# Performance work log

Measured on AMD Instinct MI355X. Metric: run time of the kernel, lower is better.

Reference implementation:

```python
import jax, jax.numpy as jnp
import numpy as np

DIM = 512
HEADS = 8
NUM_KEYS = 256
TOPK = 32
DIM_HEAD = 128
LN_EPS = 1e-5


def setup_inputs() -> dict:
    key = jax.random.key(0)
    k1, k2, k3, k4 = jax.random.split(key, 4)
    b, t = 2, 1024
    dim_query = DIM_HEAD * HEADS * 2
    x = jax.random.normal(k1, (b, t, DIM), dtype=jnp.float32)
    # nn.Linear(dim, dim_query, bias=False): weight (dim_query, dim), default kaiming-ish; use scaled normal
    Wq = jax.random.normal(k2, (dim_query, DIM), dtype=jnp.float32) / np.sqrt(DIM)
    # keys: (heads, num_keys, 2, dim_head), std = 1/sqrt(dim_head)
    keys = jax.random.normal(k3, (HEADS, NUM_KEYS, 2, DIM_HEAD), dtype=jnp.float32) / np.sqrt(DIM_HEAD)
    # values: (num_keys**2, dim), std = 1/sqrt(dim)
    values = jax.random.normal(k4, (NUM_KEYS ** 2, DIM), dtype=jnp.float32) / np.sqrt(DIM)
    ln_gamma = jnp.ones((DIM_HEAD,), dtype=jnp.float32)
    ln_beta = jnp.zeros((DIM_HEAD,), dtype=jnp.float32)
    return {"x": x, "Wq": Wq, "keys": keys, "values": values,
            "ln_gamma": ln_gamma, "ln_beta": ln_beta}


def reference(x, Wq, keys, values, ln_gamma, ln_beta):
    b, t, _ = x.shape
    h, n, _, d = keys.shape  # (heads, num_keys, 2, dim_head)
    k = TOPK

    # queries: 'b t (p h d)' -> (b, t, 2, h, d)
    q = jnp.einsum('btc,qc->btq', x, Wq).reshape(b, t, 2, h, d)

    # LayerNorm over dim_head (use_layernorm=True path)
    mu = q.mean(axis=-1, keepdims=True)
    var = q.var(axis=-1, keepdims=True)
    q = (q - mu) * jax.lax.rsqrt(var + LN_EPS) * ln_gamma + ln_beta

    # dots: 'p b t h d, h n p d -> b t h p n'
    dots = jnp.einsum('btphd,hnpd->bthpn', q, keys)

    # top-k per sub-key half: (b, t, h, 2, k)
    scores, indices = jax.lax.top_k(dots, k)
    sx, sy = scores[..., 0, :], scores[..., 1, :]
    ix, iy = indices[..., 0, :], indices[..., 1, :]

    # outer combination -> (b, t, h, k*k)
    all_scores = (sx[..., :, None] + sy[..., None, :]).reshape(b, t, h, k * k)
    all_indices = (ix[..., :, None] * n + iy[..., None, :]).reshape(b, t, h, k * k)

    final_scores, final_idx = jax.lax.top_k(all_scores, k)  # (b, t, h, k)
    value_indices = jnp.take_along_axis(all_indices, final_idx, axis=-1)
    attn = jax.nn.softmax(final_scores, axis=-1)

    vi = value_indices.reshape(b * t, h * k)
    w = attn.reshape(b * t, h * k)

    # EmbeddingBag(mode='sum') with per-sample weights
    gathered = values[vi]                      # (bt, hk, dim)
    out = jnp.einsum('nkd,nk->nd', gathered, w)
    return out.reshape(b, t, -1)
```

## Files before the change

kernel.cpp:

```cpp
#include <hip/hip_runtime.h>
#include <math.h>

#define DQ 2048
#define CDIM 512
#define NKEYS 256
#define KSEL 32

__device__ __forceinline__ bool rank_before(float as, int ai, float bs, int bi) {
  return (as > bs) || (as == bs && ai < bi);
}
static __device__ __forceinline__ float bf2f(unsigned int u) {
  union { unsigned int i; float f; } v; v.i = u << 16; return v.f;
}
static __device__ __forceinline__ unsigned int f2bf(float f) {
  union { float f; unsigned int i; } v; v.f = f;
  unsigned int r = v.i + 0x7fffu + ((v.i >> 16) & 1u);
  return r >> 16;
}

__global__ __launch_bounds__(256) void qgemm_ln(
    const float* __restrict__ X, const float* __restrict__ W,
    const float* __restrict__ gamma, const float* __restrict__ beta,
    float* __restrict__ Q) {
  __shared__ float As[16 * 68];
  __shared__ float Bs[16 * 132];
  const int tid = threadIdx.x;
  const int m0 = blockIdx.x * 64, n0 = blockIdx.y * 128;
  const int tx = tid & 15, ty = tid >> 4;
  const int am = tid >> 2, ak = (tid & 3) * 4;
  const int bn = tid >> 1, bk = (tid & 1) * 8;
  float acc[4][8] = {};
  float4 av  = *(const float4*)&X[(size_t)(m0 + am) * CDIM + ak];
  float4 bv0 = *(const float4*)&W[(size_t)(n0 + bn) * CDIM + bk];
  float4 bv1 = *(const float4*)&W[(size_t)(n0 + bn) * CDIM + bk + 4];
  for (int kt = 0; kt < CDIM; kt += 16) {
    __syncthreads();
    As[(ak + 0) * 68 + am] = av.x; As[(ak + 1) * 68 + am] = av.y;
    As[(ak + 2) * 68 + am] = av.z; As[(ak + 3) * 68 + am] = av.w;
    Bs[(bk + 0) * 132 + bn] = bv0.x; Bs[(bk + 1) * 132 + bn] = bv0.y;
    Bs[(bk + 2) * 132 + bn] = bv0.z; Bs[(bk + 3) * 132 + bn] = bv0.w;
    Bs[(bk + 4) * 132 + bn] = bv1.x; Bs[(bk + 5) * 132 + bn] = bv1.y;
    Bs[(bk + 6) * 132 + bn] = bv1.z; Bs[(bk + 7) * 132 + bn] = bv1.w;
    __syncthreads();
    if (kt + 16 < CDIM) {
      av  = *(const float4*)&X[(size_t)(m0 + am) * CDIM + kt + 16 + ak];
      bv0 = *(const float4*)&W[(size_t)(n0 + bn) * CDIM + kt + 16 + bk];
      bv1 = *(const float4*)&W[(size_t)(n0 + bn) * CDIM + kt + 16 + bk + 4];
    }
    #pragma unroll
    for (int kk = 0; kk < 16; ++kk) {
      float4 a4  = *(const float4*)&As[kk * 68 + ty * 4];
      float4 b4a = *(const float4*)&Bs[kk * 132 + tx * 8];
      float4 b4b = *(const float4*)&Bs[kk * 132 + tx * 8 + 4];
      const float ar[4] = {a4.x, a4.y, a4.z, a4.w};
      const float br[8] = {b4a.x, b4a.y, b4a.z, b4a.w, b4b.x, b4b.y, b4b.z, b4b.w};
      #pragma unroll
      for (int i = 0; i < 4; ++i)
        #pragma unroll
        for (int j = 0; j < 8; ++j)
          acc[i][j] += ar[i] * br[j];
    }
  }
  float g[8], bta[8];
  #pragma unroll
  for (int j = 0; j < 8; ++j) { g[j] = gamma[tx * 8 + j]; bta[j] = beta[tx * 8 + j]; }
  #pragma unroll
  for (int i = 0; i < 4; ++i) {
    float s = 0.f, sq = 0.f;
    #pragma unroll
    for (int j = 0; j < 8; ++j) { s += acc[i][j]; sq += acc[i][j] * acc[i][j]; }
    #pragma unroll
    for (int m = 1; m < 16; m <<= 1) {
      s += __shfl_xor(s, m, 64);
      sq += __shfl_xor(sq, m, 64);
    }
    float mean = s * (1.0f / 128.0f);
    float var = sq * (1.0f / 128.0f) - mean * mean;
    float rs = 1.0f / sqrtf(var + 1e-5f);
    float o[8];
    #pragma unroll
    for (int j = 0; j < 8; ++j) o[j] = (acc[i][j] - mean) * rs * g[j] + bta[j];
    float* dst = &Q[(size_t)(m0 + ty * 4 + i) * DQ + n0 + tx * 8];
    *(float4*)dst = make_float4(o[0], o[1], o[2], o[3]);
    *(float4*)(dst + 4) = make_float4(o[4], o[5], o[6], o[7]);
  }
}

__global__ __launch_bounds__(512, 5) void dots_sel(
    const float* __restrict__ Q, const float* __restrict__ keys,
    float* __restrict__ s1s, int* __restrict__ s1i) {
  const int hp = blockIdx.x;
  const int chunk = blockIdx.y;
  const int h = hp >> 1, p = hp & 1;
  const int t0 = chunk * 32;
  __shared__ float Qs[32 * 132];
  __shared__ float Bs[16 * 260];
  const int tid = threadIdx.x;
  const int w = tid >> 6, lane = tid & 63;
  {
    const int tok = tid >> 4, d0 = (tid & 15) * 8;
    const float* src = &Q[(size_t)(t0 + tok) * DQ + p * 1024 + h * 128 + d0];
    *(float4*)&Qs[tok * 132 + d0] = *(const float4*)src;
    *(float4*)&Qs[tok * 132 + d0 + 4] = *(const float4*)(src + 4);
  }
  const int bn = tid >> 1, bkh = (tid & 1) * 8;
  const float* kbase = keys + ((size_t)(h * NKEYS + bn) * 2 + p) * 128;
  float acc[4][4] = {};
  float4 b0 = *(const float4*)&kbase[bkh];
  float4 b1 = *(const float4*)&kbase[bkh + 4];
  for (int kt = 0; kt < 128; kt += 16) {
    __syncthreads();
    Bs[(bkh + 0) * 260 + bn] = b0.x; Bs[(bkh + 1) * 260 + bn] = b0.y;
    Bs[(bkh + 2) * 260 + bn] = b0.z; Bs[(bkh + 3) * 260 + bn] = b0.w;
    Bs[(bkh + 4) * 260 + bn] = b1.x; Bs[(bkh + 5) * 260 + bn] = b1.y;
    Bs[(bkh + 6) * 260 + bn] = b1.z; Bs[(bkh + 7) * 260 + bn] = b1.w;
    __syncthreads();
    if (kt + 16 < 128) {
      b0 = *(const float4*)&kbase[kt + 16 + bkh];
      b1 = *(const float4*)&kbase[kt + 16 + bkh + 4];
    }
    #pragma unroll
    for (int k4 = 0; k4 < 16; k4 += 4) {
      float4 a0 = *(const float4*)&Qs[(w * 4 + 0) * 132 + kt + k4];
      float4 a1 = *(const float4*)&Qs[(w * 4 + 1) * 132 + kt + k4];
      float4 a2 = *(const float4*)&Qs[(w * 4 + 2) * 132 + kt + k4];
      float4 a3 = *(const float4*)&Qs[(w * 4 + 3) * 132 + kt + k4];
      const float a0r[4] = {a0.x, a0.y, a0.z, a0.w};
      const float a1r[4] = {a1.x, a1.y, a1.z, a1.w};
      const float a2r[4] = {a2.x, a2.y, a2.z, a2.w};
      const float a3r[4] = {a3.x, a3.y, a3.z, a3.w};
      #pragma unroll
      for (int kk = 0; kk < 4; ++kk) {
        float4 b4 = *(const float4*)&Bs[(k4 + kk) * 260 + lane * 4];
        const float br[4] = {b4.x, b4.y, b4.z, b4.w};
        #pragma unroll
        for (int j = 0; j < 4; ++j) {
          acc[0][j] += a0r[kk] * br[j];
          acc[1][j] += a1r[kk] * br[j];
          acc[2][j] += a2r[kk] * br[j];
          acc[3][j] += a3r[kk] * br[j];
        }
      }
    }
  }
  #define CE1(S, I, a, b, dd)                                                  \
    {                                                                          \
      bool sw_ = (dd) ? rank_before(S[a], I[a], S[b], I[b])                    \
                      : rank_before(S[b], I[b], S[a], I[a]);                   \
      if (sw_) {                                                               \
        float ts_ = S[a]; S[a] = S[b]; S[b] = ts_;                             \
        int ti_ = I[a]; I[a] = I[b]; I[b] = ti_;                               \
      }                                                                        \
    }
  #define CEP(a, b, dd) { CE1(sA, iA, a, b, dd) CE1(sB, iB, a, b, dd) }
  #define CROSSP(L, dd)                                                        \
    {                                                                          \
      bool amHigh = (lane & (L)) != 0;                                         \
      bool flip = amHigh != (dd);                                              \
      _Pragma("unroll")                                                        \
      for (int r = 0; r < 4; ++r) {                                            \
        float osA = __shfl_xor(sA[r], (L), 64);                                \
        int oiA = __shfl_xor(iA[r], (L), 64);                                  \
        float osB = __shfl_xor(sB[r], (L), 64);                                \
        int oiB = __shfl_xor(iB[r], (L), 64);                                  \
        bool tA = rank_before(osA, oiA, sA[r], iA[r]) != flip;                 \
        if (tA) { sA[r] = osA; iA[r] = oiA; }                                  \
        bool tB = rank_before(osB, oiB, sB[r], iB[r]) != flip;                 \
        if (tB) { sB[r] = osB; iB[r] = oiB; }                                  \
      }                                                                        \
    }
  #pragma unroll
  for (int ii = 0; ii < 4; ii += 2) {
    float sA[4], sB[4]; int iA[4], iB[4];
    #pragma unroll
    for (int r = 0; r < 4; ++r) {
      sA[r] = acc[ii][r];     iA[r] = lane * 4 + r;
      sB[r] = acc[ii + 1][r]; iB[r] = lane * 4 + r;
    }
    CEP(0, 1, false); CEP(2, 3, true);
    {
      bool dd = (lane & 1) != 0;
      CEP(0, 2, dd); CEP(1, 3, dd); CEP(0, 1, dd); CEP(2, 3, dd);
    }
    #pragma unroll
    for (int K = 8; K <= 256; K <<= 1) {
      bool dd = (lane & (K >> 2)) != 0;
      #pragma unroll
      for (int L = K >> 3; L >= 1; L >>= 1) CROSSP(L, dd);
      CEP(0, 2, dd); CEP(1, 3, dd); CEP(0, 1, dd); CEP(2, 3, dd);
    }
    const int instA = (t0 + w * 4 + ii) * 16 + hp;
    const int instB = instA + 16;
    if (lane < 8) {
      *(float4*)&s1s[(size_t)instA * KSEL + lane * 4] = make_float4(sA[0], sA[1], sA[2], sA[3]);
      *(int4*)&s1i[(size_t)instA * KSEL + lane * 4] = make_int4(iA[0], iA[1], iA[2], iA[3]);
      *(float4*)&s1s[(size_t)instB * KSEL + lane * 4] = make_float4(sB[0], sB[1], sB[2], sB[3]);
      *(int4*)&s1i[(size_t)instB * KSEL + lane * 4] = make_int4(iB[0], iB[1], iB[2], iB[3]);
    }
  }
  #undef CE1
  #undef CEP
  #undef CROSSP
}

__constant__ unsigned short slot_ij[128] = {
  0,1,2,3,4,5,6,7,8,9,10,11,12,13,14,15,16,17,18,19,20,21,22,23,24,25,26,27,28,29,30,31,
  32,33,34,35,36,37,38,39,40,41,42,43,44,45,46,47,
  64,65,66,67,68,69,70,71,72,73,
  96,97,98,99,100,101,102,103,
  128,129,130,131,132,133,
  160,161,162,163,164,
  192,193,194,195,
  224,225,226,227,
  256,257,258,
  288,289,290,
  320,321, 352,353, 384,385, 416,417, 448,449, 480,481,
  512,544,576,608,640,672,704,736,768,800,832,864,896,928,960,992,
  0xFFFF,0xFFFF,0xFFFF,0xFFFF,0xFFFF,0xFFFF,0xFFFF,0xFFFF,0xFFFF
};

__global__ __launch_bounds__(256) void stage2_kernel(
    const float* __restrict__ s1s, const int* __restrict__ s1i,
    float* __restrict__ wgt, int* __restrict__ vidx) {
  const int th = blockIdx.x * 4 + (threadIdx.x >> 6);
  const int lane = threadIdx.x & 63;
  const int bx = th * 64;
  const int by = bx + 32;
  float s[2]; int id[2];
  #pragma unroll
  for (int r = 0; r < 2; ++r) {
    int sl = slot_ij[lane * 2 + r];
    if (sl != 0xFFFF) {
      s[r] = s1s[bx + (sl >> 5)] + s1s[by + (sl & 31)];
      id[r] = sl;
    } else {
      s[r] = -INFINITY; id[r] = 0x7fffffff;
    }
  }
  #define CE2(dd)                                                              \
    {                                                                          \
      bool sw = (dd) ? rank_before(s[0], id[0], s[1], id[1])                   \
                     : rank_before(s[1], id[1], s[0], id[0]);                  \
      if (sw) {                                                                \
        float ts = s[0]; s[0] = s[1]; s[1] = ts;                               \
        int ti = id[0]; id[0] = id[1]; id[1] = ti;                             \
      }                                                                        \
    }
  #define CROSS2(L, dd)                                                        \
    {                                                                          \
      bool amHigh = (lane & (L)) != 0;                                         \
      bool flip = amHigh != (dd);                                              \
      _Pragma("unroll")                                                        \
      for (int r = 0; r < 2; ++r) {                                            \
        float os = __shfl_xor(s[r], (L), 64);                                  \
        int oi = __shfl_xor(id[r], (L), 64);                                   \
        bool take = rank_before(os, oi, s[r], id[r]) != flip;                  \
        if (take) { s[r] = os; id[r] = oi; }                                   \
      }                                                                        \
    }
  { bool dd = (lane & 1) != 0; CE2(dd); }
  #pragma unroll
  for (int K = 4; K <= 128; K <<= 1) {
    bool dd = (lane & (K >> 1)) != 0;
    #pragma unroll
    for (int L = K >> 2; L >= 1; L >>= 1) CROSS2(L, dd);
    CE2(dd);
  }
  #undef CE2
  #undef CROSS2
  float smax = __shfl(s[0], 0, 64);
  float e0 = 0.f, e1 = 0.f;
  if (lane < 16) { e0 = expf(s[0] - smax); e1 = expf(s[1] - smax); }
  float part = e0 + e1;
  #pragma unroll
  for (int m = 1; m < 16; m <<= 1) part += __shfl_xor(part, m, 64);
  if (lane < 16) {
    int f0 = id[0], f1 = id[1];
    int vi0 = s1i[bx + (f0 >> 5)] * NKEYS + s1i[by + (f0 & 31)];
    int vi1 = s1i[bx + (f1 >> 5)] * NKEYS + s1i[by + (f1 & 31)];
    wgt[(size_t)th * KSEL + lane * 2] = e0 / part;
    wgt[(size_t)th * KSEL + lane * 2 + 1] = e1 / part;
    vidx[(size_t)th * KSEL + lane * 2] = vi0;
    vidx[(size_t)th * KSEL + lane * 2 + 1] = vi1;
  }
}

__global__ __launch_bounds__(256) void convert_values(
    const float* __restrict__ values, unsigned int* __restrict__ vbf) {
  const size_t g = ((size_t)blockIdx.x * 256 + threadIdx.x) * 8;
  float4 a = *(const float4*)(values + g);
  float4 b = *(const float4*)(values + g + 4);
  uint4 pk;
  pk.x = f2bf(a.x) | (f2bf(a.y) << 16);
  pk.y = f2bf(a.z) | (f2bf(a.w) << 16);
  pk.z = f2bf(b.x) | (f2bf(b.y) << 16);
  pk.w = f2bf(b.z) | (f2bf(b.w) << 16);
  *(uint4*)(vbf + g / 2) = pk;
}

__global__ __launch_bounds__(256) void gather_bf16(
    const float* __restrict__ wgt, const int* __restrict__ vidx,
    const unsigned short* __restrict__ vbf, float* __restrict__ out) {
  const int t = blockIdx.x;
  const int tid = threadIdx.x, w = tid >> 6, lane = tid & 63;
  __shared__ float ws_[256];
  __shared__ int vs_[256];
  __shared__ float part[4 * 520];
  ws_[tid] = wgt[(size_t)t * 256 + tid];
  vs_[tid] = vidx[(size_t)t * 256 + tid];
  __syncthreads();
  float acc[8] = {};
  const int c0 = lane * 8;
  #pragma unroll 1
  for (int phase = 0; phase < 4; ++phase) {
    for (int e = w; e < 256; e += 4) {
      const int row = vs_[e];
      if ((row >> 14) != phase) continue;
      const float wv = ws_[e];
      uint4 pk = *(const uint4*)(vbf + (size_t)row * CDIM + c0);
      acc[0] += wv * bf2f(pk.x & 0xffff); acc[1] += wv * bf2f(pk.x >> 16);
      acc[2] += wv * bf2f(pk.y & 0xffff); acc[3] += wv * bf2f(pk.y >> 16);
      acc[4] += wv * bf2f(pk.z & 0xffff); acc[5] += wv * bf2f(pk.z >> 16);
      acc[6] += wv * bf2f(pk.w & 0xffff); acc[7] += wv * bf2f(pk.w >> 16);
    }
  }
  #pragma unroll
  for (int j = 0; j < 8; j += 4)
    *(float4*)&part[w * 520 + c0 + j] =
        make_float4(acc[j], acc[j + 1], acc[j + 2], acc[j + 3]);
  __syncthreads();
  const int c2 = tid * 2;
  float r0 = part[c2] + part[520 + c2] + part[1040 + c2] + part[1560 + c2];
  float r1 = part[c2 + 1] + part[520 + c2 + 1] + part[1040 + c2 + 1] + part[1560 + c2 + 1];
  *(float2*)(out + (size_t)t * CDIM + c2) = make_float2(r0, r1);
}

__global__ __launch_bounds__(256) void gather_kernel(
    const float* __restrict__ wgt, const int* __restrict__ vidx,
    const float* __restrict__ values, float* __restrict__ out) {
  const int tp = blockIdx.x;
  const int tid = threadIdx.x;
  __shared__ float ws_[512];
  __shared__ int vs_[512];
  ws_[tid] = wgt[(size_t)tp * 512 + tid];
  ws_[tid + 256] = wgt[(size_t)tp * 512 + tid + 256];
  vs_[tid] = vidx[(size_t)tp * 512 + tid];
  vs_[tid + 256] = vidx[(size_t)tp * 512 + tid + 256];
  __syncthreads();
  const int sub = tid >> 7;
  const int c4 = (tid & 127) * 4;
  const float* wp = &ws_[sub * 256];
  const int* vp = &vs_[sub * 256];
  float4 a = make_float4(0.f, 0.f, 0.f, 0.f);
  #pragma unroll 4
  for (int e = 0; e < 256; ++e) {
    float4 vv = *(const float4*)(values + (size_t)vp[e] * CDIM + c4);
    float wv = wp[e];
    a.x += wv * vv.x; a.y += wv * vv.y; a.z += wv * vv.z; a.w += wv * vv.w;
  }
  *(float4*)(out + (size_t)(tp * 2 + sub) * CDIM + c4) = a;
}

extern "C" void kernel_launch(void* const* d_in, const int* in_sizes, int n_in,
                              void* d_out, int out_size, void* d_ws, size_t ws_size,
                              hipStream_t stream) {
  const float* X      = (const float*)d_in[0];
  const float* W      = (const float*)d_in[1];
  const float* keys   = (const float*)d_in[2];
  const float* values = (const float*)d_in[3];
  const float* gamma  = (const float*)d_in[4];
  const float* beta   = (const float*)d_in[5];
  char* ws = (char*)d_ws;
  float* s1s = (float*)(ws);
  int*   s1i = (int*)  (ws + (4u << 20));
  float* wgt = (float*)(ws + (8u << 20));
  int*   vix = (int*)  (ws + (10u << 20));
  float* Q   = (float*)(ws + (12u << 20));
  unsigned int* vbf = (unsigned int*)(ws + (12u << 20));

  const bool bf16_path = ws_size >= (76u << 20);

  qgemm_ln<<<dim3(32, 16), 256, 0, stream>>>(X, W, gamma, beta, Q);
  dots_sel<<<dim3(16, 64), 512, 0, stream>>>(Q, keys, s1s, s1i);
  stage2_kernel<<<4096, 256, 0, stream>>>(s1s, s1i, wgt, vix);
  if (bf16_path) {
    convert_values<<<16384, 256, 0, stream>>>(values, vbf);
    gather_bf16<<<2048, 256, 0, stream>>>(wgt, vix, (const unsigned short*)vbf, (float*)d_out);
  } else {
    gather_kernel<<<1024, 256, 0, stream>>>(wgt, vix, values, (float*)d_out);
  }
}
```

Baseline: 454.9 us.

## Pre-transpose keys and read them directly from global memory in dots_sel

```diff
diff --git a/kernel.cpp b/kernel.cpp
--- a/kernel.cpp
+++ b/kernel.cpp
@@ -86,15 +86,46 @@
   }
 }
 
+__global__ __launch_bounds__(256) void transpose_keys(
+    const float* __restrict__ keys, float* __restrict__ keysT) {
+  __shared__ float tile[64 * 129];
+  const int hp = blockIdx.x, h = hp >> 1, p = hp & 1;
+  const int n0 = blockIdx.y * 64;
+  {
+    const int n = threadIdx.x >> 2;
+    const int d0 = (threadIdx.x & 3) * 32;
+    const float* src = &keys[(((size_t)h * NKEYS + n0 + n) * 2 + p) * 128 + d0];
+    #pragma unroll
+    for (int j = 0; j < 32; j += 4) {
+      float4 v = *(const float4*)(src + j);
+      tile[n * 129 + d0 + j + 0] = v.x;
+      tile[n * 129 + d0 + j + 1] = v.y;
+      tile[n * 129 + d0 + j + 2] = v.z;
+      tile[n * 129 + d0 + j + 3] = v.w;
+    }
+  }
+  __syncthreads();
+  {
+    const int d = threadIdx.x >> 1;
+    const int nh = (threadIdx.x & 1) * 32;
+    float* dst = &keysT[((size_t)hp * 128 + d) * NKEYS + n0 + nh];
+    #pragma unroll
+    for (int j = 0; j < 32; j += 4) {
+      float4 o = make_float4(tile[(nh + j + 0) * 129 + d], tile[(nh + j + 1) * 129 + d],
+                             tile[(nh + j + 2) * 129 + d], tile[(nh + j + 3) * 129 + d]);
+      *(float4*)(dst + j) = o;
+    }
+  }
+}
+
 __global__ __launch_bounds__(512, 5) void dots_sel(
-    const float* __restrict__ Q, const float* __restrict__ keys,
+    const float* __restrict__ Q, const float* __restrict__ keysT,
     float* __restrict__ s1s, int* __restrict__ s1i) {
   const int hp = blockIdx.x;
   const int chunk = blockIdx.y;
   const int h = hp >> 1, p = hp & 1;
   const int t0 = chunk * 32;
   __shared__ float Qs[32 * 132];
-  __shared__ float Bs[16 * 260];
   const int tid = threadIdx.x;
   const int w = tid >> 6, lane = tid & 63;
   {
@@ -103,43 +134,29 @@
     *(float4*)&Qs[tok * 132 + d0] = *(const float4*)src;
     *(float4*)&Qs[tok * 132 + d0 + 4] = *(const float4*)(src + 4);
   }
-  const int bn = tid >> 1, bkh = (tid & 1) * 8;
-  const float* kbase = keys + ((size_t)(h * NKEYS + bn) * 2 + p) * 128;
+  __syncthreads();
+  const float* kT = keysT + (size_t)hp * 128 * NKEYS + lane * 4;
   float acc[4][4] = {};
-  float4 b0 = *(const float4*)&kbase[bkh];
-  float4 b1 = *(const float4*)&kbase[bkh + 4];
-  for (int kt = 0; kt < 128; kt += 16) {
-    __syncthreads();
-    Bs[(bkh + 0) * 260 + bn] = b0.x; Bs[(bkh + 1) * 260 + bn] = b0.y;
-    Bs[(bkh + 2) * 260 + bn] = b0.z; Bs[(bkh + 3) * 260 + bn] = b0.w;
-    Bs[(bkh + 4) * 260 + bn] = b1.x; Bs[(bkh + 5) * 260 + bn] = b1.y;
-    Bs[(bkh + 6) * 260 + bn] = b1.z; Bs[(bkh + 7) * 260 + bn] = b1.w;
-    __syncthreads();
-    if (kt + 16 < 128) {
-      b0 = *(const float4*)&kbase[kt + 16 + bkh];
-      b1 = *(const float4*)&kbase[kt + 16 + bkh + 4];
-    }
-    #pragma unroll
-    for (int k4 = 0; k4 < 16; k4 += 4) {
-      float4 a0 = *(const float4*)&Qs[(w * 4 + 0) * 132 + kt + k4];
-      float4 a1 = *(const float4*)&Qs[(w * 4 + 1) * 132 + kt + k4];
-      float4 a2 = *(const float4*)&Qs[(w * 4 + 2) * 132 + kt + k4];
-      float4 a3 = *(const float4*)&Qs[(w * 4 + 3) * 132 + kt + k4];
-      const float a0r[4] = {a0.x, a0.y, a0.z, a0.w};
-      const float a1r[4] = {a1.x, a1.y, a1.z, a1.w};
-      const float a2r[4] = {a2.x, a2.y, a2.z, a2.w};
-      const float a3r[4] = {a3.x, a3.y, a3.z, a3.w};
+  #pragma unroll 2
+  for (int kt = 0; kt < 128; kt += 4) {
+    float4 a0 = *(const float4*)&Qs[(w * 4 + 0) * 132 + kt];
+    float4 a1 = *(const float4*)&Qs[(w * 4 + 1) * 132 + kt];
+    float4 a2 = *(const float4*)&Qs[(w * 4 + 2) * 132 + kt];
+    float4 a3 = *(const float4*)&Qs[(w * 4 + 3) * 132 + kt];
+    const float a0r[4] = {a0.x, a0.y, a0.z, a0.w};
+    const float a1r[4] = {a1.x, a1.y, a1.z, a1.w};
+    const float a2r[4] = {a2.x, a2.y, a2.z, a2.w};
+    const float a3r[4] = {a3.x, a3.y, a3.z, a3.w};
+    #pragma unroll
+    for (int kk = 0; kk < 4; ++kk) {
+      float4 b4 = *(const float4*)&kT[(size_t)(kt + kk) * NKEYS];
+      const float br[4] = {b4.x, b4.y, b4.z, b4.w};
       #pragma unroll
-      for (int kk = 0; kk < 4; ++kk) {
-        float4 b4 = *(const float4*)&Bs[(k4 + kk) * 260 + lane * 4];
-        const float br[4] = {b4.x, b4.y, b4.z, b4.w};
-        #pragma unroll
-        for (int j = 0; j < 4; ++j) {
-          acc[0][j] += a0r[kk] * br[j];
-          acc[1][j] += a1r[kk] * br[j];
-          acc[2][j] += a2r[kk] * br[j];
-          acc[3][j] += a3r[kk] * br[j];
-        }
+      for (int j = 0; j < 4; ++j) {
+        acc[0][j] += a0r[kk] * br[j];
+        acc[1][j] += a1r[kk] * br[j];
+        acc[2][j] += a2r[kk] * br[j];
+        acc[3][j] += a3r[kk] * br[j];
       }
     }
   }
@@ -376,12 +393,14 @@
   float* wgt = (float*)(ws + (8u << 20));
   int*   vix = (int*)  (ws + (10u << 20));
   float* Q   = (float*)(ws + (12u << 20));
+  float* kT  = (float*)(ws + (28u << 20));
   unsigned int* vbf = (unsigned int*)(ws + (12u << 20));
 
   const bool bf16_path = ws_size >= (76u << 20);
 
+  transpose_keys<<<dim3(16, 4), 256, 0, stream>>>(keys, kT);
   qgemm_ln<<<dim3(32, 16), 256, 0, stream>>>(X, W, gamma, beta, Q);
-  dots_sel<<<dim3(16, 64), 512, 0, stream>>>(Q, keys, s1s, s1i);
+  dots_sel<<<dim3(16, 64), 512, 0, stream>>>(Q, kT, s1s, s1i);
   stage2_kernel<<<4096, 256, 0, stream>>>(s1s, s1i, wgt, vix);
   if (bf16_path) {
     convert_values<<<16384, 256, 0, stream>>>(values, vbf);
```

Measured after the change: 452.8 us. No clear change (-0.5%).
